# Kernel optimization log

Measured on AMD Instinct MI355X. Metric: run time of the kernel, lower is better.

## Reference

```python
import jax, jax.numpy as jnp
import numpy as np

B, S, H, NH = 16, 384, 1024, 16
HD = H // NH  # head_dim = 64

def setup_inputs() -> dict:
    key = jax.random.key(0)
    k1, k2, k3 = jax.random.split(key, 3)
    activation = jax.random.normal(k1, (B, S, H), dtype=jnp.float32)
    attention_mask = jnp.zeros((B, 1, 1, S), dtype=jnp.float32)  # additive mask
    qkv_weight = jax.random.normal(k2, (H, 3 * H), dtype=jnp.float32) * 0.02
    qkv_bias = jax.random.normal(k3, (3 * H,), dtype=jnp.float32) * 0.02
    return {"activation": activation, "attention_mask": attention_mask,
            "qkv_weight": qkv_weight, "qkv_bias": qkv_bias}

def reference(activation, attention_mask, qkv_weight, qkv_bias):
    # op1: fused QKV projection
    qkv = activation @ qkv_weight + qkv_bias            # [B,S,3H]
    q, k, v = jnp.split(qkv, 3, axis=-1)                # each [B,S,H]
    # op2-6: split heads -> [B,NH,S,HD]
    def heads(x):
        return x.reshape(B, S, NH, HD).transpose(0, 2, 1, 3)
    q, k, v = heads(q), heads(k), heads(v)
    # op7: QK^T
    scores = jnp.einsum('bhqd,bhkd->bhqk', q, k)        # [B,NH,S,S]
    # op8: scale + mask + softmax (scale applied to scores, then additive mask)
    scale = 1.0 / np.sqrt(HD).astype(np.float32)
    probs = jax.nn.softmax(scores * scale + attention_mask, axis=-1)
    # op9: weighted V
    out = jnp.einsum('bhqk,bhkd->bhqd', probs, v)       # [B,NH,S,HD]
    # op10: concat heads
    return out.transpose(0, 2, 1, 3).reshape(B, S, H)
```

## Files before the change

kernel.cpp:

```cpp
#include <hip/hip_runtime.h>
#include <hip/hip_bf16.h>

#define BB 16
#define SS 384
#define HH 1024
#define NH 16
#define HD 64
#define MM (BB*SS)
#define KK HH
#define N3 (3*HH)

typedef float f32x4 __attribute__((ext_vector_type(4)));
typedef __bf16 bf16x8 __attribute__((ext_vector_type(8)));
typedef unsigned short us8 __attribute__((ext_vector_type(8)));
typedef unsigned short us4 __attribute__((ext_vector_type(4)));

__device__ __forceinline__ void gload_lds16(const void* g, void* l) {
    __builtin_amdgcn_global_load_lds(
        (const __attribute__((address_space(1))) void*)g,
        (__attribute__((address_space(3))) void*)l, 16, 0, 0);
}

__device__ __forceinline__ unsigned short f2b(float f) {
    __bf16 h = (__bf16)f;
    return __builtin_bit_cast(unsigned short, h);
}

__global__ __launch_bounds__(256) void cvt_x(const float4* __restrict__ in,
                                             us4* __restrict__ out, int n4) {
    int i = blockIdx.x * 256 + threadIdx.x;
    if (i < n4) {
        float4 v = in[i];
        us4 o;
        o.x = f2b(v.x); o.y = f2b(v.y); o.z = f2b(v.z); o.w = f2b(v.w);
        out[i] = o;
    }
}

__global__ __launch_bounds__(256) void cvt_w(const float* __restrict__ Wf,
                                             __bf16* __restrict__ WT) {
    __shared__ float tile[32][33];
    const int n0 = blockIdx.x * 32, k0 = blockIdx.y * 32;
    const int t = threadIdx.x;
    const int tj = t & 31, ti = t >> 5;
#pragma unroll
    for (int p = 0; p < 4; ++p) {
        int i = p * 8 + ti;
        tile[i][tj] = Wf[(size_t)(k0 + i) * N3 + n0 + tj];
    }
    __syncthreads();
#pragma unroll
    for (int p = 0; p < 4; ++p) {
        int jj = p * 8 + ti;
        WT[(size_t)(n0 + jj) * KK + k0 + tj] = (__bf16)tile[tj][jj];
    }
}

__global__ __launch_bounds__(256) void qkv_gemm(const __bf16* __restrict__ Xb,
                                                const __bf16* __restrict__ WT,
                                                const float* __restrict__ bias,
                                                __bf16* __restrict__ QKb,
                                                __bf16* __restrict__ VTg) {
    __shared__ __bf16 As[128 * 32];
    __shared__ __bf16 Bs[128 * 32];
    const int t = threadIdx.x;
    const int w = t >> 6, lane = t & 63;
    const int wr = w >> 1, wc = w & 1;
    const int l15 = lane & 15, lg = lane >> 4;
    const int m0 = blockIdx.y * 128, n0 = blockIdx.x * 128;

    f32x4 acc[4][4] = {};

    for (int k0 = 0; k0 < KK; k0 += 32) {
#pragma unroll
        for (int i = 0; i < 2; ++i) {
            int slab = w * 2 + i;
            int row = slab * 16 + (lane >> 2);
            int ck = lane & 3;
            gload_lds16(Xb + (size_t)(m0 + row) * KK + k0 + ck * 8, &As[slab * 512]);
            gload_lds16(WT + (size_t)(n0 + row) * KK + k0 + ck * 8, &Bs[slab * 512]);
        }
        __syncthreads();

        bf16x8 a[4];
#pragma unroll
        for (int i = 0; i < 4; ++i) {
            int row = wr * 64 + i * 16 + l15;
            a[i] = *(const bf16x8*)&As[row * 32 + lg * 8];
        }
#pragma unroll
        for (int j = 0; j < 4; ++j) {
            int row = wc * 64 + j * 16 + l15;
            bf16x8 bv = *(const bf16x8*)&Bs[row * 32 + lg * 8];
#pragma unroll
            for (int i = 0; i < 4; ++i)
                acc[i][j] = __builtin_amdgcn_mfma_f32_16x16x32_bf16(a[i], bv, acc[i][j], 0, 0, 0);
        }
        __syncthreads();
    }

#pragma unroll
    for (int j = 0; j < 4; ++j) {
        int c = n0 + wc * 64 + j * 16 + l15;
        float bv = bias[c];
#pragma unroll
        for (int i = 0; i < 4; ++i) {
#pragma unroll
            for (int r = 0; r < 4; ++r) {
                int rr = m0 + wr * 64 + i * 16 + lg * 4 + r;
                float v = acc[i][j][r] + bv;
                if (c < 2048) {
                    QKb[(size_t)rr * 2048 + c] = (__bf16)v;
                } else {
                    int d = c & 63;
                    int hh = (c - 2048) >> 6;
                    int bb = rr / SS;
                    int s = rr - bb * SS;
                    VTg[((size_t)(bb * NH + hh) * HD + d) * SS + s] = (__bf16)v;
                }
            }
        }
    }
}

#define KLOFF 0
#define VTOFF 49152
#define PLOFF 98304
#define QLOFF 147456
#define MKOFF 155648
#define SMEMSZ 157184

__global__ __launch_bounds__(256) void attn(const __bf16* __restrict__ QKb,
                                            const __bf16* __restrict__ VTg,
                                            const float* __restrict__ maskg,
                                            float* __restrict__ out) {
    extern __shared__ char smem[];
    const int head = blockIdx.x;
    const int b = head >> 4, h = head & 15;
    const int t = threadIdx.x;
    const int w = t >> 6, lane = t & 63;
    const int l15 = lane & 15, lg = lane >> 4;

    for (int it = 0; it < 12; ++it) {
        int slot = it * 256 + t;
        int row = slot >> 3, ck = slot & 7;
        us8 v = *(const us8*)&QKb[(size_t)(b * SS + row) * 2048 + 1024 + h * 64 + ck * 8];
        int byte = (row * 128 + ck * 16) ^ ((row & 7) << 4);
        *(us8*)(smem + KLOFF + byte) = v;
    }
    for (int it = 0; it < 12; ++it) {
        int slot = it * 256 + t;
        int d = slot / 48, ck = slot - d * 48;
        us8 v = *(const us8*)&VTg[((size_t)head * HD + d) * SS + ck * 8];
        int byte = (d * 768 + ck * 16) ^ ((d & 7) << 4);
        *(us8*)(smem + VTOFF + byte) = v;
    }
    for (int s = t; s < SS; s += 256)
        ((float*)(smem + MKOFF))[s] = maskg[b * SS + s];
    __syncthreads();

    for (int q0 = 0; q0 < SS; q0 += 64) {
        for (int it = 0; it < 2; ++it) {
            int slot = it * 256 + t;
            int row = slot >> 3, ck = slot & 7;
            us8 v = *(const us8*)&QKb[(size_t)(b * SS + q0 + row) * 2048 + h * 64 + ck * 8];
            int byte = (row * 128 + ck * 16) ^ ((row & 7) << 4);
            *(us8*)(smem + QLOFF + byte) = v;
        }
        __syncthreads();

        f32x4 acc[24];
#pragma unroll
        for (int f = 0; f < 24; ++f) acc[f] = f32x4{0.f, 0.f, 0.f, 0.f};
        bf16x8 aq[2];
        {
            int row = w * 16 + l15;
#pragma unroll
            for (int st = 0; st < 2; ++st)
                aq[st] = *(const bf16x8*)(smem + QLOFF +
                          ((row * 128 + st * 64 + lg * 16) ^ ((row & 7) << 4)));
        }
#pragma unroll
        for (int f = 0; f < 24; ++f) {
            int row = f * 16 + l15;
#pragma unroll
            for (int st = 0; st < 2; ++st) {
                bf16x8 kb = *(const bf16x8*)(smem + KLOFF +
                             ((row * 128 + st * 64 + lg * 16) ^ ((row & 7) << 4)));
                acc[f] = __builtin_amdgcn_mfma_f32_16x16x32_bf16(aq[st], kb, acc[f], 0, 0, 0);
            }
        }

        const float* mrow = (const float*)(smem + MKOFF);
        float mx[4] = {-1e30f, -1e30f, -1e30f, -1e30f};
#pragma unroll
        for (int f = 0; f < 24; ++f) {
            float mk = mrow[f * 16 + l15];
#pragma unroll
            for (int r = 0; r < 4; ++r) {
                float v = acc[f][r] * 0.125f + mk;
                acc[f][r] = v;
                mx[r] = fmaxf(mx[r], v);
            }
        }
#pragma unroll
        for (int off = 8; off >= 1; off >>= 1)
#pragma unroll
            for (int r = 0; r < 4; ++r) mx[r] = fmaxf(mx[r], __shfl_xor(mx[r], off, 64));
        float sm[4] = {0.f, 0.f, 0.f, 0.f};
#pragma unroll
        for (int f = 0; f < 24; ++f)
#pragma unroll
            for (int r = 0; r < 4; ++r) {
                float p = __expf(acc[f][r] - mx[r]);
                acc[f][r] = p;
                sm[r] += p;
            }
#pragma unroll
        for (int off = 8; off >= 1; off >>= 1)
#pragma unroll
            for (int r = 0; r < 4; ++r) sm[r] += __shfl_xor(sm[r], off, 64);
        float inv[4];
#pragma unroll
        for (int r = 0; r < 4; ++r) inv[r] = 1.f / sm[r];

#pragma unroll
        for (int f = 0; f < 24; ++f)
#pragma unroll
            for (int r = 0; r < 4; ++r) {
                int row = w * 16 + lg * 4 + r;
                int col = f * 16 + l15;
                int byte = (row * 768 + col * 2) ^ ((row & 7) << 4);
                *(__bf16*)(smem + PLOFF + byte) = (__bf16)acc[f][r];
            }
        __syncthreads();

        f32x4 o[4] = {};
#pragma unroll
        for (int st = 0; st < 12; ++st) {
            int prow = w * 16 + l15;
            bf16x8 pa = *(const bf16x8*)(smem + PLOFF +
                         ((prow * 768 + st * 64 + lg * 16) ^ ((prow & 7) << 4)));
#pragma unroll
            for (int j = 0; j < 4; ++j) {
                int d = j * 16 + l15;
                bf16x8 vb = *(const bf16x8*)(smem + VTOFF +
                             ((d * 768 + st * 64 + lg * 16) ^ ((d & 7) << 4)));
                o[j] = __builtin_amdgcn_mfma_f32_16x16x32_bf16(pa, vb, o[j], 0, 0, 0);
            }
        }

#pragma unroll
        for (int j = 0; j < 4; ++j)
#pragma unroll
            for (int r = 0; r < 4; ++r) {
                int qrow = q0 + w * 16 + lg * 4 + r;
                out[(size_t)(b * SS + qrow) * HH + h * 64 + j * 16 + l15] =
                    o[j][r] * inv[r];
            }
    }
}

extern "C" void kernel_launch(void* const* d_in, const int* in_sizes, int n_in,
                              void* d_out, int out_size, void* d_ws, size_t ws_size,
                              hipStream_t stream) {
    const float* act  = (const float*)d_in[0];
    const float* mask = (const float*)d_in[1];
    const float* wq   = (const float*)d_in[2];
    const float* bias = (const float*)d_in[3];

    char* ws = (char*)d_ws;
    __bf16* Xb  = (__bf16*)(ws);
    __bf16* WT  = (__bf16*)(ws + 12582912);
    __bf16* QKb = (__bf16*)(ws + 18874368);
    __bf16* VTg = (__bf16*)(ws + 44040192);

    cvt_x<<<(MM * KK / 4 + 255) / 256, 256, 0, stream>>>((const float4*)act, (us4*)Xb, MM * KK / 4);
    cvt_w<<<dim3(N3 / 32, KK / 32), 256, 0, stream>>>(wq, WT);
    qkv_gemm<<<dim3(N3 / 128, MM / 128), 256, 0, stream>>>(Xb, WT, bias, QKb, VTg);

    (void)hipFuncSetAttribute((const void*)attn, hipFuncAttributeMaxDynamicSharedMemorySize, SMEMSZ);
    attn<<<BB * NH, 256, SMEMSZ, stream>>>(QKb, VTg, mask, (float*)d_out);
}
```

Baseline: 133.1 us.

## Double GEMM K-tile, swizzle LDS layout, and remap blocks per XCD

The QKV GEMM now stages 64-wide K slabs instead of 32, halving the number of barrier-separated iterations. An XOR swizzle on the 16-byte chunks avoids LDS bank conflicts on the wider rows. The grid becomes 1D with a mapping that gives each XCD a contiguous 12x12 tile region, to improve L2 reuse of A and B panels. LDS use doubles per block, which may reduce occupancy.

```diff
diff --git a/kernel.cpp b/kernel.cpp
--- a/kernel.cpp
+++ b/kernel.cpp
@@ -61,40 +61,58 @@
                                                 const float* __restrict__ bias,
                                                 __bf16* __restrict__ QKb,
                                                 __bf16* __restrict__ VTg) {
-    __shared__ __bf16 As[128 * 32];
-    __shared__ __bf16 Bs[128 * 32];
+    __shared__ __bf16 As[128 * 64];
+    __shared__ __bf16 Bs[128 * 64];
     const int t = threadIdx.x;
     const int w = t >> 6, lane = t & 63;
     const int wr = w >> 1, wc = w & 1;
     const int l15 = lane & 15, lg = lane >> 4;
-    const int m0 = blockIdx.y * 128, n0 = blockIdx.x * 128;
+
+    const int bid = blockIdx.x;
+    const int xcd = bid & 7, loc = bid >> 3;
+    const int by = (xcd >> 1) * 12 + (loc / 12);
+    const int bx = (xcd & 1) * 12 + (loc % 12);
+    const int m0 = by * 128, n0 = bx * 128;
+
+    const int sc = (lane & 7) ^ (lane >> 3);
+    const __bf16* Ap[4];
+    const __bf16* Bp[4];
+#pragma unroll
+    for (int i = 0; i < 4; ++i) {
+        int row = (w * 4 + i) * 8 + (lane >> 3);
+        Ap[i] = Xb + (size_t)(m0 + row) * KK + sc * 8;
+        Bp[i] = WT + (size_t)(n0 + row) * KK + sc * 8;
+    }
+    const int swA = l15 & 7;
 
     f32x4 acc[4][4] = {};
 
-    for (int k0 = 0; k0 < KK; k0 += 32) {
-#pragma unroll
-        for (int i = 0; i < 2; ++i) {
-            int slab = w * 2 + i;
-            int row = slab * 16 + (lane >> 2);
-            int ck = lane & 3;
-            gload_lds16(Xb + (size_t)(m0 + row) * KK + k0 + ck * 8, &As[slab * 512]);
-            gload_lds16(WT + (size_t)(n0 + row) * KK + k0 + ck * 8, &Bs[slab * 512]);
+    for (int k0 = 0; k0 < KK; k0 += 64) {
+#pragma unroll
+        for (int i = 0; i < 4; ++i) {
+            gload_lds16(Ap[i] + k0, &As[(w * 4 + i) * 512]);
+            gload_lds16(Bp[i] + k0, &Bs[(w * 4 + i) * 512]);
         }
         __syncthreads();
 
-        bf16x8 a[4];
-#pragma unroll
-        for (int i = 0; i < 4; ++i) {
-            int row = wr * 64 + i * 16 + l15;
-            a[i] = *(const bf16x8*)&As[row * 32 + lg * 8];
-        }
-#pragma unroll
-        for (int j = 0; j < 4; ++j) {
-            int row = wc * 64 + j * 16 + l15;
-            bf16x8 bv = *(const bf16x8*)&Bs[row * 32 + lg * 8];
-#pragma unroll
-            for (int i = 0; i < 4; ++i)
-                acc[i][j] = __builtin_amdgcn_mfma_f32_16x16x32_bf16(a[i], bv, acc[i][j], 0, 0, 0);
+#pragma unroll
+        for (int kk = 0; kk < 2; ++kk) {
+            bf16x8 a[4];
+#pragma unroll
+            for (int i = 0; i < 4; ++i) {
+                int row = wr * 64 + i * 16 + l15;
+                int ch = (kk * 4 + lg) ^ swA;
+                a[i] = *(const bf16x8*)&As[row * 64 + ch * 8];
+            }
+#pragma unroll
+            for (int j = 0; j < 4; ++j) {
+                int row = wc * 64 + j * 16 + l15;
+                int ch = (kk * 4 + lg) ^ swA;
+                bf16x8 bv = *(const bf16x8*)&Bs[row * 64 + ch * 8];
+#pragma unroll
+                for (int i = 0; i < 4; ++i)
+                    acc[i][j] = __builtin_amdgcn_mfma_f32_16x16x32_bf16(a[i], bv, acc[i][j], 0, 0, 0);
+            }
         }
         __syncthreads();
     }
@@ -277,7 +295,7 @@
 
     cvt_x<<<(MM * KK / 4 + 255) / 256, 256, 0, stream>>>((const float4*)act, (us4*)Xb, MM * KK / 4);
     cvt_w<<<dim3(N3 / 32, KK / 32), 256, 0, stream>>>(wq, WT);
-    qkv_gemm<<<dim3(N3 / 128, MM / 128), 256, 0, stream>>>(Xb, WT, bias, QKb, VTg);
+    qkv_gemm<<<dim3(1152), 256, 0, stream>>>(Xb, WT, bias, QKb, VTg);
 
     (void)hipFuncSetAttribute((const void*)attn, hipFuncAttributeMaxDynamicSharedMemorySize, SMEMSZ);
     attn<<<BB * NH, 256, SMEMSZ, stream>>>(QKb, VTg, mask, (float*)d_out);
```

Result: slower. 138.5 us (+4.0%).

## Use single-wave 64x64 GEMM blocks to drop workgroup barriers in QKV projection

Applied to the files above, without the earlier changes.

The QKV GEMM changes from 256-thread blocks computing 128x128 tiles to single-wavefront blocks computing 64x64 tiles. With only one wave per block, both __syncthreads calls are replaced by explicit s_waitcnt on the LDS and global-load counters, removing workgroup barrier cost. The trade-off is that each block now loads its A and B tiles for only one wave, so operand reuse per LDS tile falls and global/L2 traffic roughly doubles. The grid grows fourfold to keep the GPU occupied.

```diff
diff --git a/kernel.cpp b/kernel.cpp
--- a/kernel.cpp
+++ b/kernel.cpp
@@ -56,58 +56,55 @@
     }
 }
 
-__global__ __launch_bounds__(256) void qkv_gemm(const __bf16* __restrict__ Xb,
-                                                const __bf16* __restrict__ WT,
-                                                const float* __restrict__ bias,
-                                                __bf16* __restrict__ QKb,
-                                                __bf16* __restrict__ VTg) {
-    __shared__ __bf16 As[128 * 32];
-    __shared__ __bf16 Bs[128 * 32];
-    const int t = threadIdx.x;
-    const int w = t >> 6, lane = t & 63;
-    const int wr = w >> 1, wc = w & 1;
+__global__ __launch_bounds__(64, 4) void qkv_gemm(const __bf16* __restrict__ Xb,
+                                                  const __bf16* __restrict__ WT,
+                                                  const float* __restrict__ bias,
+                                                  __bf16* __restrict__ QKb,
+                                                  __bf16* __restrict__ VTg) {
+    __shared__ __bf16 As[64 * 32];
+    __shared__ __bf16 Bs[64 * 32];
+    const int lane = threadIdx.x;
     const int l15 = lane & 15, lg = lane >> 4;
-    const int m0 = blockIdx.y * 128, n0 = blockIdx.x * 128;
+    const int m0 = blockIdx.y * 64, n0 = blockIdx.x * 64;
+
+    const int srow = lane >> 2, sch = (lane & 3) * 8;
+    const __bf16* Ap = Xb + (size_t)(m0 + srow) * KK + sch;
+    const __bf16* Bp = WT + (size_t)(n0 + srow) * KK + sch;
 
     f32x4 acc[4][4] = {};
 
     for (int k0 = 0; k0 < KK; k0 += 32) {
-#pragma unroll
-        for (int i = 0; i < 2; ++i) {
-            int slab = w * 2 + i;
-            int row = slab * 16 + (lane >> 2);
-            int ck = lane & 3;
-            gload_lds16(Xb + (size_t)(m0 + row) * KK + k0 + ck * 8, &As[slab * 512]);
-            gload_lds16(WT + (size_t)(n0 + row) * KK + k0 + ck * 8, &Bs[slab * 512]);
-        }
-        __syncthreads();
+        asm volatile("s_waitcnt lgkmcnt(0)" ::: "memory");
+#pragma unroll
+        for (int s = 0; s < 4; ++s) {
+            gload_lds16(Ap + (size_t)(s * 16) * KK + k0, &As[s * 512]);
+            gload_lds16(Bp + (size_t)(s * 16) * KK + k0, &Bs[s * 512]);
+        }
+        asm volatile("s_waitcnt vmcnt(0)" ::: "memory");
+        __builtin_amdgcn_sched_barrier(0);
 
         bf16x8 a[4];
 #pragma unroll
-        for (int i = 0; i < 4; ++i) {
-            int row = wr * 64 + i * 16 + l15;
-            a[i] = *(const bf16x8*)&As[row * 32 + lg * 8];
-        }
+        for (int i = 0; i < 4; ++i)
+            a[i] = *(const bf16x8*)&As[(i * 16 + l15) * 32 + lg * 8];
 #pragma unroll
         for (int j = 0; j < 4; ++j) {
-            int row = wc * 64 + j * 16 + l15;
-            bf16x8 bv = *(const bf16x8*)&Bs[row * 32 + lg * 8];
+            bf16x8 bv = *(const bf16x8*)&Bs[(j * 16 + l15) * 32 + lg * 8];
 #pragma unroll
             for (int i = 0; i < 4; ++i)
                 acc[i][j] = __builtin_amdgcn_mfma_f32_16x16x32_bf16(a[i], bv, acc[i][j], 0, 0, 0);
         }
-        __syncthreads();
     }
 
 #pragma unroll
     for (int j = 0; j < 4; ++j) {
-        int c = n0 + wc * 64 + j * 16 + l15;
+        int c = n0 + j * 16 + l15;
         float bv = bias[c];
 #pragma unroll
         for (int i = 0; i < 4; ++i) {
 #pragma unroll
             for (int r = 0; r < 4; ++r) {
-                int rr = m0 + wr * 64 + i * 16 + lg * 4 + r;
+                int rr = m0 + i * 16 + lg * 4 + r;
                 float v = acc[i][j][r] + bv;
                 if (c < 2048) {
                     QKb[(size_t)rr * 2048 + c] = (__bf16)v;
@@ -277,7 +274,7 @@
 
     cvt_x<<<(MM * KK / 4 + 255) / 256, 256, 0, stream>>>((const float4*)act, (us4*)Xb, MM * KK / 4);
     cvt_w<<<dim3(N3 / 32, KK / 32), 256, 0, stream>>>(wq, WT);
-    qkv_gemm<<<dim3(N3 / 128, MM / 128), 256, 0, stream>>>(Xb, WT, bias, QKb, VTg);
+    qkv_gemm<<<dim3(N3 / 64, MM / 64), 64, 0, stream>>>(Xb, WT, bias, QKb, VTg);
 
     (void)hipFuncSetAttribute((const void*)attn, hipFuncAttributeMaxDynamicSharedMemorySize, SMEMSZ);
     attn<<<BB * NH, 256, SMEMSZ, stream>>>(QKb, VTg, mask, (float*)d_out);
```

Result: slower. 150.4 us (+13.0%).
